# Kernel tuning notes

Measured on AMD Instinct MI355X. Metric: run time of the kernel, lower is better.

## Reference

```python
import jax, jax.numpy as jnp
import numpy as np

B, S, H, Dh = 16, 577, 16, 64
D = H * Dh
DT = 0.01      # resonance_kwargs['dt']
BETA = 4.0     # inverse temperature for phase-coherence readout


def setup_inputs() -> dict:
    key = jax.random.key(0)
    ks = jax.random.split(key, 12)
    n = lambda k, shape, s: jax.random.normal(k, shape, jnp.float32) * s
    return {
        'x': n(ks[0], (B, S, D), 1.0),
        'Wq': n(ks[1], (H, Dh, Dh), 0.08), 'bq': jnp.zeros((H, Dh), jnp.float32),
        'Wk': n(ks[2], (H, Dh, Dh), 0.08), 'bk': jnp.zeros((H, Dh), jnp.float32),
        'Wv': n(ks[3], (H, Dh, Dh), 0.08), 'bv': jnp.zeros((H, Dh), jnp.float32),
        'Womega': n(ks[4], (H, Dh), 0.08), 'bomega': jnp.zeros((H,), jnp.float32),
        'Wtheta': n(ks[5], (H, Dh), 0.08), 'btheta': jnp.zeros((H,), jnp.float32),
        'mu': jnp.ones((H,), jnp.float32),                      # Stuart-Landau growth rate
        'kappa': jnp.full((H,), 0.5, jnp.float32),              # coupling strength
        'alpha': jnp.full((H,), 0.1, jnp.float32),              # Sakaguchi phase lag
        'mix_logit': jnp.full((H,), float(np.log(9.0)), jnp.float32),  # sigmoid -> 0.9 hybrid_mix_init
        'band_logits': jnp.zeros((H, 4), jnp.float32),          # spectral gating, 4 bands
        'Wo': n(ks[6], (D, D), 0.02), 'bo': jnp.zeros((D,), jnp.float32),
        'n_sim_steps': 10,
    }


def reference(x, Wq, bq, Wk, bk, Wv, bv, Womega, bomega, Wtheta, btheta,
              mu, kappa, alpha, mix_logit, band_logits, Wo, bo, n_sim_steps):
    b, s, dm = x.shape
    h, dh = Wq.shape[0], Wq.shape[1]
    # split into per-head slices: [B, H, S, dh]
    xh = x.reshape(b, s, h, dh).transpose(0, 2, 1, 3)
    xh = jnp.nan_to_num(xh, nan=0.0, posinf=0.0, neginf=0.0)
    q = jnp.einsum('bhsd,hde->bhse', xh, Wq) + bq[None, :, None, :]
    k = jnp.einsum('bhsd,hde->bhse', xh, Wk) + bk[None, :, None, :]
    v = jnp.einsum('bhsd,hde->bhse', xh, Wv) + bv[None, :, None, :]
    scale = 1.0 / jnp.sqrt(jnp.float32(dh))
    K = jnp.einsum('bhse,bhte->bhst', q, k) * scale            # coupling kernel / vanilla scores
    # per-token natural frequency and initial phase
    omega = jnp.einsum('bhsd,hd->bhs', xh, Womega) + bomega[None, :, None]
    theta0 = jnp.einsum('bhsd,hd->bhs', xh, Wtheta) + btheta[None, :, None]
    zr0, zi0 = jnp.cos(theta0), jnp.sin(theta0)                # z = r e^{i theta}, r0 = 1
    ca = jnp.cos(alpha)[None, :, None]
    sa = jnp.sin(alpha)[None, :, None]
    Kc = (kappa[None, :, None, None] / s) * K                  # normalized coupling matrix
    mu_b = mu[None, :, None]
    # Stuart-Landau + Kuramoto-Sakaguchi vector field:
    # dz = (mu - |z|^2 + i*omega) z + e^{-i alpha} (Kc @ z)
    def f(zr, zi):
        ur = jnp.einsum('bhst,bht->bhs', Kc, zr)
        ui = jnp.einsum('bhst,bht->bhs', Kc, zi)
        cr = ca * ur + sa * ui
        ci = ca * ui - sa * ur
        g = mu_b - (zr * zr + zi * zi)
        return g * zr - omega * zi + cr, g * zi + omega * zr + ci
    # Heun (predictor-corrector) integration, n_sim_steps steps
    def step(carry, _):
        zr, zi = carry
        d1r, d1i = f(zr, zi)
        d2r, d2i = f(zr + DT * d1r, zi + DT * d1i)
        return (zr + 0.5 * DT * (d1r + d2r), zi + 0.5 * DT * (d1i + d2i)), None
    (zr, zi), _ = jax.lax.scan(step, (zr0, zi0), None, length=n_sim_steps)
    # phase-coherence readout: Re(z_i conj(z_j)) = r_i r_j cos(theta_i - theta_j)
    coher = jnp.einsum('bhs,bht->bhst', zr, zr) + jnp.einsum('bhs,bht->bhst', zi, zi)
    A_res = jax.nn.softmax(BETA * coher, axis=-1)
    # spectral gating of V: 4 bands over the head dim
    gate = jax.nn.sigmoid(band_logits)                          # [H, 4]
    gate_full = jnp.repeat(gate, dh // gate.shape[1], axis=-1)  # [H, dh]
    y_res = jnp.einsum('bhst,bhtd->bhsd', A_res, v * gate_full[None, :, None, :])
    # vanilla QK^T attention branch (hybrid readout)
    y_van = jnp.einsum('bhst,bhtd->bhsd', jax.nn.softmax(K, axis=-1), v)
    mix = jax.nn.sigmoid(mix_logit)[None, :, None, None]
    y = mix * y_res + (1.0 - mix) * y_van
    y = y.transpose(0, 2, 1, 3).reshape(b, s, dm)
    return y @ Wo + bo                                          # base_attn dense/out_proj
```

## Files before the change

kernel.cpp:

```cpp
#include <hip/hip_runtime.h>
#include <hip/hip_bf16.h>

#define S_ 577
#define B_ 16
#define H_ 16
#define DH 64
#define DM 1024
#define BH_ 256
#define DT_ 0.01f
#define BETA_ 4.0f
#define SCALE_ 0.125f
#define SPP 292
#define KPR 293
#define SPW2 37
#define L2E 1.44269504f
#define OFFV2 (4.0f * L2E)
#define OFFR2 (6.0f * L2E)

typedef float f32x4 __attribute__((ext_vector_type(4)));
typedef short s16x8 __attribute__((ext_vector_type(8)));
typedef short s16x4 __attribute__((ext_vector_type(4)));

__device__ inline short f2bf(float x) {
    unsigned b = __builtin_bit_cast(unsigned, x);
    b += 0x7fffu + ((b >> 16) & 1u);
    return (short)(b >> 16);
}
__device__ inline float bf2f(short s) {
    unsigned u = ((unsigned)(unsigned short)s) << 16;
    return __builtin_bit_cast(float, u);
}
__device__ inline float ex2(float x) {
    float r;
    asm("v_exp_f32 %0, %1" : "=v"(r) : "v"(x));
    return r;
}
__device__ inline int vswz(int row) { return (((row >> 3) ^ row) & 7) << 3; }

__global__ __launch_bounds__(512) void k_proj(
    const float* __restrict__ x,
    const float* __restrict__ Wq, const float* __restrict__ bq,
    const float* __restrict__ Wk, const float* __restrict__ bk,
    const float* __restrict__ Wv, const float* __restrict__ bv,
    const float* __restrict__ Wom, const float* __restrict__ bom,
    const float* __restrict__ Wth, const float* __restrict__ bth,
    short* __restrict__ qh, short* __restrict__ kh, short* __restrict__ vh,
    float* __restrict__ om, float* __restrict__ zp)
{
    __shared__ __align__(16) short WqT[64*64], WkT[64*64], WvT[64*64];
    __shared__ __align__(16) short X_l[128*64];
    __shared__ float Wom_l[64], Wth_l[64];

    int bh = blockIdx.x, b = bh >> 4, h = bh & 15;
    int tid = threadIdx.x, w = tid >> 6, lane = tid & 63;
    int c = lane & 15, g = lane >> 4;

    {
        int d = tid >> 3, e0 = (tid & 7) << 3;
        const float* pq = Wq + (size_t)h*4096 + d*64 + e0;
        const float* pk = Wk + (size_t)h*4096 + d*64 + e0;
        const float* pv = Wv + (size_t)h*4096 + d*64 + e0;
        float4 q0 = *(const float4*)pq, q1 = *(const float4*)(pq + 4);
        float4 k0 = *(const float4*)pk, k1 = *(const float4*)(pk + 4);
        float4 v0 = *(const float4*)pv, v1 = *(const float4*)(pv + 4);
        float qv[8] = {q0.x,q0.y,q0.z,q0.w,q1.x,q1.y,q1.z,q1.w};
        float kv[8] = {k0.x,k0.y,k0.z,k0.w,k1.x,k1.y,k1.z,k1.w};
        float vv[8] = {v0.x,v0.y,v0.z,v0.w,v1.x,v1.y,v1.z,v1.w};
        #pragma unroll
        for (int j = 0; j < 8; ++j) {
            int e = e0 + j;
            int off = e*64 + (d ^ ((e&7)<<3));
            WqT[off] = f2bf(qv[j]);
            WkT[off] = f2bf(kv[j]);
            WvT[off] = f2bf(vv[j]);
        }
    }
    if (tid < 64) { Wom_l[tid] = Wom[h*64 + tid]; Wth_l[tid] = Wth[h*64 + tid]; }

    float bqv[4], bkv[4], bvv[4];
    #pragma unroll
    for (int e4 = 0; e4 < 4; ++e4) {
        bqv[e4] = bq[h*64 + e4*16 + c];
        bkv[e4] = bk[h*64 + e4*16 + c];
        bvv[e4] = bv[h*64 + e4*16 + c];
    }
    float bomv = bom[h], bthv = bth[h];

    const size_t xbase = (size_t)b*S_*DM + (size_t)h*DH;

    for (int t5 = 0; t5 < 5; ++t5) {
        int s0 = t5 * 128;
        __syncthreads();
        #pragma unroll
        for (int i = 0; i < 2; ++i) {
            int cid = tid + 512*i;
            int row = cid >> 3, ch = cid & 7;
            int s = s0 + row;
            float xv[8];
            if (s < S_) {
                const float* px = x + xbase + (size_t)s*DM + ch*8;
                float4 a0 = *(const float4*)px, a1 = *(const float4*)(px + 4);
                xv[0]=a0.x; xv[1]=a0.y; xv[2]=a0.z; xv[3]=a0.w;
                xv[4]=a1.x; xv[5]=a1.y; xv[6]=a1.z; xv[7]=a1.w;
                #pragma unroll
                for (int j = 0; j < 8; ++j) if (!isfinite(xv[j])) xv[j] = 0.f;
            } else {
                #pragma unroll
                for (int j = 0; j < 8; ++j) xv[j] = 0.f;
            }
            s16x8 xb;
            #pragma unroll
            for (int j = 0; j < 8; ++j) xb[j] = f2bf(xv[j]);
            *(s16x8*)&X_l[row*64 + ((ch*8) ^ ((row&7)<<3))] = xb;
            float po = 0.f, pt = 0.f;
            #pragma unroll
            for (int j = 0; j < 8; ++j) {
                po = fmaf(xv[j], Wom_l[ch*8 + j], po);
                pt = fmaf(xv[j], Wth_l[ch*8 + j], pt);
            }
            po += __shfl_xor(po, 1, 64); pt += __shfl_xor(pt, 1, 64);
            po += __shfl_xor(po, 2, 64); pt += __shfl_xor(pt, 2, 64);
            po += __shfl_xor(po, 4, 64); pt += __shfl_xor(pt, 4, 64);
            if (ch == 0 && s < S_) {
                om[(size_t)bh*S_ + s] = po + bomv;
                float si, co;
                sincosf(pt + bthv, &si, &co);
                reinterpret_cast<float2*>(zp)[(size_t)bh*S_ + s] = make_float2(co, si);
            }
        }
        __syncthreads();
        int arow = w*16 + c;
        s16x8 xa0 = *(const s16x8*)&X_l[arow*64 + ((g*8)      ^ ((arow&7)<<3))];
        s16x8 xa1 = *(const s16x8*)&X_l[arow*64 + ((g*8 + 32) ^ ((arow&7)<<3))];

        const short* WT[3] = {WqT, WkT, WvT};
        short* dst[3] = {qh, kh, vh};
        #pragma unroll
        for (int o = 0; o < 3; ++o) {
            f32x4 acc[4];
            #pragma unroll
            for (int e4 = 0; e4 < 4; ++e4) {
                int brow = e4*16 + c;
                s16x8 b0 = *(const s16x8*)&WT[o][brow*64 + ((g*8)      ^ ((brow&7)<<3))];
                s16x8 b1 = *(const s16x8*)&WT[o][brow*64 + ((g*8 + 32) ^ ((brow&7)<<3))];
                f32x4 a = {0.f,0.f,0.f,0.f};
                a = __builtin_amdgcn_mfma_f32_16x16x32_bf16(xa0, b0, a, 0, 0, 0);
                a = __builtin_amdgcn_mfma_f32_16x16x32_bf16(xa1, b1, a, 0, 0, 0);
                acc[e4] = a;
            }
            float* bias = (o == 0) ? bqv : (o == 1) ? bkv : bvv;
            #pragma unroll
            for (int r = 0; r < 4; ++r) {
                int s = s0 + w*16 + 4*g + r;
                if (s < S_) {
                    s16x4 pk;
                    pk[0] = f2bf(acc[0][r] + bias[0]);
                    pk[1] = f2bf(acc[1][r] + bias[1]);
                    pk[2] = f2bf(acc[2][r] + bias[2]);
                    pk[3] = f2bf(acc[3][r] + bias[3]);
                    *(s16x4*)(dst[o] + (size_t)bh*S_*DH + (size_t)s*DH + c*4) = pk;
                }
            }
        }
    }
}

__global__ __launch_bounds__(1024) void k_ode(
    const short* __restrict__ qh, const short* __restrict__ kh,
    const float* __restrict__ om,
    const float* __restrict__ mu, const float* __restrict__ kappa,
    const float* __restrict__ alpha, const int* __restrict__ nsim,
    float* __restrict__ zp)
{
    __shared__ __align__(16) unsigned kp_l[64*KPR];
    __shared__ __align__(16) short    q_l[S_*64];
    __shared__ __align__(16) float2   z_l[584];
    __shared__ __align__(16) float2   z1_l[584];
    __shared__ __align__(16) float2   kz_s[8][64];

    int bh = blockIdx.x, h = bh & 15;
    int tid = threadIdx.x, w = tid >> 6, lane = tid & 63;
    const short* kg = kh + (size_t)bh*S_*DH;
    const short* qg = qh + (size_t)bh*S_*DH;
    float2* zpg = reinterpret_cast<float2*>(zp) + (size_t)bh*S_;
    const float* omg = om + (size_t)bh*S_;

    for (int i = tid; i < 584; i += 1024) {
        z_l[i] = (i < S_) ? zpg[i] : make_float2(0.f, 0.f);
        z1_l[i] = make_float2(0.f, 0.f);
    }
    {
        int e0 = (tid & 7) * 8;
        for (int sp = tid >> 3; sp < SPP; sp += 128) {
            int sA = 2*sp, sB = 2*sp + 1;
            s16x8 ka = {0,0,0,0,0,0,0,0}, kb = ka;
            if (sA < S_) ka = *(const s16x8*)(kg + (size_t)sA*DH + e0);
            if (sB < S_) kb = *(const s16x8*)(kg + (size_t)sB*DH + e0);
            #pragma unroll
            for (int j = 0; j < 8; ++j)
                kp_l[(e0+j)*KPR + sp] =
                    ((unsigned)(unsigned short)ka[j]) |
                    (((unsigned)(unsigned short)kb[j]) << 16);
        }
    }
    for (int cid = tid; cid < S_*8; cid += 1024) {
        int s = cid >> 3, c = cid & 7;
        s16x8 v = *(const s16x8*)(qg + (size_t)s*DH + c*8);
        *(s16x8*)&q_l[s*64 + ((c*8) ^ ((s&7)<<3))] = v;
    }
    int i8 = lane >> 3, d0 = (lane & 7) << 3;
    int s0 = w * SPW2;
    float om_r[5];
    #pragma unroll
    for (int m2 = 0; m2 < 5; ++m2) {
        int li = i8 + 8*m2, s = s0 + li;
        om_r[m2] = (li < SPW2 && s < S_) ? omg[s] : 0.f;
    }
    float ca = cosf(alpha[h]), sa = sinf(alpha[h]);
    float muv = mu[h];
    float cc = kappa[h] * SCALE_ / (float)S_;
    int NT = nsim[0];
    int sp0 = (w * SPP) >> 4, spE = ((w + 1) * SPP) >> 4;
    __syncthreads();

    for (int ev = 0; ev < 2*NT; ++ev) {
        bool second = ev & 1;
        const float2* zin = second ? z1_l : z_l;
        float ar = 0.f, ai = 0.f, br = 0.f, bi = 0.f;
        for (int sp = sp0; sp < spE; ++sp) {
            unsigned kv = kp_l[lane*KPR + sp];
            float4 zz = *reinterpret_cast<const float4*>(&zin[2*sp]);
            float klo = __builtin_bit_cast(float, kv << 16);
            float khi = __builtin_bit_cast(float, kv & 0xffff0000u);
            ar = fmaf(klo, zz.x, ar); ai = fmaf(klo, zz.y, ai);
            br = fmaf(khi, zz.z, br); bi = fmaf(khi, zz.w, bi);
        }
        float2 part = make_float2(ar + br, ai + bi);
        if (w < 8) kz_s[w][lane] = part;
        __syncthreads();
        if (w >= 8) {
            float2 t = kz_s[w - 8][lane];
            t.x += part.x; t.y += part.y;
            kz_s[w - 8][lane] = t;
        }
        __syncthreads();
        float sr = 0.f, si = 0.f;
        #pragma unroll
        for (int w2 = 0; w2 < 8; ++w2) {
            float2 t = kz_s[w2][lane];
            sr += t.x; si += t.y;
        }
        float kzr[8], kzi[8];
        #pragma unroll
        for (int j = 0; j < 8; ++j) {
            kzr[j] = __shfl(sr, d0 + j, 64);
            kzi[j] = __shfl(si, d0 + j, 64);
        }
        #pragma unroll
        for (int m2 = 0; m2 < 5; ++m2) {
            int li = i8 + 8*m2, s = s0 + li;
            bool act = (li < SPW2) && (s < S_);
            int sq = (s <= S_-1) ? s : S_-1;
            s16x8 qv = *(const s16x8*)&q_l[sq*64 + (d0 ^ ((sq&7)<<3))];
            float ur = 0.f, ui = 0.f;
            #pragma unroll
            for (int j = 0; j < 8; ++j) {
                float qf = bf2f(qv[j]);
                ur = fmaf(qf, kzr[j], ur);
                ui = fmaf(qf, kzi[j], ui);
            }
            #pragma unroll
            for (int mm = 1; mm < 8; mm <<= 1) {
                ur += __shfl_xor(ur, mm, 64);
                ui += __shfl_xor(ui, mm, 64);
            }
            if (act && d0 == 0) {
                float2 z = zin[s];
                float urc = cc*ur, uic = cc*ui;
                float cr = ca*urc + sa*uic;
                float ci = ca*uic - sa*urc;
                float g = muv - (z.x*z.x + z.y*z.y);
                float dr = fmaf(g, z.x, fmaf(-om_r[m2], z.y, cr));
                float di = fmaf(g, z.y, fmaf( om_r[m2], z.x, ci));
                float2 zb = z_l[s];
                if (!second) {
                    z1_l[s] = make_float2(fmaf(DT_, dr, z.x), fmaf(DT_, di, z.y));
                    z_l[s]  = make_float2(fmaf(0.5f*DT_, dr, zb.x), fmaf(0.5f*DT_, di, zb.y));
                } else {
                    z_l[s]  = make_float2(fmaf(0.5f*DT_, dr, zb.x), fmaf(0.5f*DT_, di, zb.y));
                }
            }
        }
        __syncthreads();
    }
    for (int i = tid; i < S_; i += 1024) zpg[i] = z_l[i];
}

__global__ __launch_bounds__(512) void k_attn(
    const short* __restrict__ qh, const short* __restrict__ kh,
    const short* __restrict__ vh, const float* __restrict__ zp,
    const float* __restrict__ mix_logit, const float* __restrict__ band_logits,
    short* __restrict__ yh)
{
    __shared__ short q_l[128*64];
    __shared__ short P1_l[8][1024];
    __shared__ short k_l2[64*64];
    __shared__ short vT_l[64*64];
    __shared__ float2 zs_l[128];
    __shared__ float2 zt_l[64];

    int blk = blockIdx.x;
    int bh = blk / 5, rc = blk - bh*5;
    int b = bh >> 4, h = bh & 15;
    int r0 = rc * 128;
    int tid = threadIdx.x, w = tid >> 6, lane = tid & 63;
    int c = lane & 15, g = lane >> 4;

    const short* qg = qh + (size_t)bh*S_*DH;
    const short* kg = kh + (size_t)bh*S_*DH;
    const short* vg = vh + (size_t)bh*S_*DH;
    const float2* zpg = (const float2*)zp + (size_t)bh*S_;

    #pragma unroll
    for (int i = 0; i < 2; ++i) {
        int cid = tid + 512*i;
        int row = cid >> 3, ch = cid & 7;
        int s = r0 + row;
        s16x8 val = {0,0,0,0,0,0,0,0};
        if (s < S_) val = *(const s16x8*)(qg + (size_t)s*DH + ch*8);
        *(s16x8*)&q_l[row*64 + ((ch*8) ^ ((row&7)<<3))] = val;
    }
    if (tid < 128) {
        float2 z = (r0 + tid < S_) ? zpg[r0 + tid] : make_float2(0.f,0.f);
        zs_l[tid] = make_float2(z.x*(BETA_*L2E), z.y*(BETA_*L2E));
    }
    __syncthreads();

    s16x8 qf0, qf1;
    {
        int row = w*16 + c;
        qf0 = *(const s16x8*)&q_l[row*64 + ((g*8)      ^ ((row&7)<<3))];
        qf1 = *(const s16x8*)&q_l[row*64 + ((g*8 + 32) ^ ((row&7)<<3))];
    }
    float2 zsr[4];
    #pragma unroll
    for (int r = 0; r < 4; ++r) zsr[r] = zs_l[w*16 + (g<<2) + r];

    f32x4 accv[4], accr[4];
    float Z_v[4], Z_r[4];
    #pragma unroll
    for (int i = 0; i < 4; ++i) {
        accv[i] = (f32x4){0.f,0.f,0.f,0.f};
        accr[i] = (f32x4){0.f,0.f,0.f,0.f};
        Z_v[i] = 0.f; Z_r[i] = 0.f;
    }

    short* P0 = &q_l[w << 10];
    short* P1 = &P1_l[w][0];

    for (int tt = 0; tt < 10; ++tt) {
        int t0g = tt * 64;
        __syncthreads();
        {
            int row = tid >> 3, ch = tid & 7;
            int t = t0g + row;
            s16x8 val = {0,0,0,0,0,0,0,0};
            if (t < S_) val = *(const s16x8*)(kg + (size_t)t*DH + ch*8);
            *(s16x8*)&k_l2[row*64 + ((ch*8) ^ ((row&7)<<3))] = val;
        }
        {
            int tloc = tid >> 3, d0 = (tid & 7) << 3;
            int pt = ((tloc & 15) << 2) + (tloc >> 4);
            s16x8 vv = {0,0,0,0,0,0,0,0};
            if (t0g + tloc < S_) vv = *(const s16x8*)(vg + (size_t)(t0g+tloc)*DH + d0);
            #pragma unroll
            for (int j = 0; j < 8; ++j) {
                int sc = d0 + j;
                int te = ((sc & 3) << 4) + (sc >> 2);
                vT_l[te*64 + (pt ^ vswz(te))] = vv[j];
            }
        }
        if (tid < 64) zt_l[tid] = (t0g + tid < S_) ? zpg[t0g + tid] : make_float2(0.f,0.f);
        __syncthreads();

        f32x4 sv[4], sr4[4];
        #pragma unroll
        for (int sub = 0; sub < 4; ++sub) {
            int row = sub*16 + c;
            s16x8 kf0 = *(const s16x8*)&k_l2[row*64 + ((g*8)      ^ ((c&7)<<3))];
            s16x8 kf1 = *(const s16x8*)&k_l2[row*64 + ((g*8 + 32) ^ ((c&7)<<3))];
            f32x4 a = {0.f,0.f,0.f,0.f};
            a = __builtin_amdgcn_mfma_f32_16x16x32_bf16(qf0, kf0, a, 0, 0, 0);
            a = __builtin_amdgcn_mfma_f32_16x16x32_bf16(qf1, kf1, a, 0, 0, 0);
            sv[sub] = a * (SCALE_ * L2E) - OFFV2;
        }
        #pragma unroll
        for (int sub = 0; sub < 4; ++sub) {
            float2 zt = zt_l[sub*16 + c];
            #pragma unroll
            for (int r = 0; r < 4; ++r)
                sr4[sub][r] = fmaf(zsr[r].x, zt.x, fmaf(zsr[r].y, zt.y, -OFFR2));
        }
        if (t0g + 64 > S_) {
            #pragma unroll
            for (int sub = 0; sub < 4; ++sub)
                if (t0g + sub*16 + c >= S_) {
                    #pragma unroll
                    for (int r = 0; r < 4; ++r) { sv[sub][r] = -1e30f; sr4[sub][r] = -1e30f; }
                }
        }

        #pragma unroll
        for (int r = 0; r < 4; ++r) {
            int sl = (g<<2) + r;
            int pco = sl*64 + ((c*4) ^ ((sl&7)<<3));
            s16x4 pk0, pk1;
            float sumv = 0.f, sumr = 0.f;
            #pragma unroll
            for (int sub = 0; sub < 4; ++sub) {
                float pv = ex2(sv[sub][r]);
                float pr = ex2(sr4[sub][r]);
                sumv += pv; sumr += pr;
                pk0[sub] = f2bf(pv);
                pk1[sub] = f2bf(pr);
            }
            *(s16x4*)&P0[pco] = pk0;
            *(s16x4*)&P1[pco] = pk1;
            Z_v[r] += sumv;
            Z_r[r] += sumr;
        }

        #pragma unroll
        for (int hh = 0; hh < 2; ++hh) {
            int kc = g*8 + 32*hh;
            int po = c*64 + (kc ^ ((c&7)<<3));
            s16x8 pa_v = *(const s16x8*)&P0[po];
            s16x8 pa_r = *(const s16x8*)&P1[po];
            #pragma unroll
            for (int d = 0; d < 4; ++d) {
                int row = d*16 + c;
                s16x8 vf = *(const s16x8*)&vT_l[row*64 + (kc ^ vswz(row))];
                accv[d] = __builtin_amdgcn_mfma_f32_16x16x32_bf16(pa_v, vf, accv[d], 0, 0, 0);
                accr[d] = __builtin_amdgcn_mfma_f32_16x16x32_bf16(pa_r, vf, accr[d], 0, 0, 0);
            }
        }
    }

    #pragma unroll
    for (int mm = 1; mm < 16; mm <<= 1) {
        #pragma unroll
        for (int r = 0; r < 4; ++r) {
            Z_v[r] += __shfl_xor(Z_v[r], mm, 64);
            Z_r[r] += __shfl_xor(Z_r[r], mm, 64);
        }
    }

    float mixv = 1.f/(1.f + __expf(-mix_logit[h]));
    #pragma unroll
    for (int d = 0; d < 4; ++d) {
        float gate = 1.f/(1.f + __expf(-band_logits[h*4 + d]));
        #pragma unroll
        for (int r = 0; r < 4; ++r) {
            int s = r0 + w*16 + (g<<2) + r;
            if (s < S_) {
                float val = mixv*gate*(accr[d][r]/Z_r[r]) + (1.f-mixv)*(accv[d][r]/Z_v[r]);
                yh[(size_t)b*S_*DM + (size_t)s*DM + h*DH + d*16 + c] = f2bf(val);
            }
        }
    }
}

__global__ __launch_bounds__(256) void k_cvt(
    const float* __restrict__ Wo, short* __restrict__ Bt)
{
    __shared__ short tl[64][65];
    int k0 = blockIdx.x * 64, n0 = blockIdx.y * 64;
    int tid = threadIdx.x;
    int r = tid >> 2, cb = (tid & 3) * 16;
    #pragma unroll
    for (int j4 = 0; j4 < 4; ++j4) {
        float4 v = *reinterpret_cast<const float4*>(Wo + (size_t)(k0+r)*1024 + n0 + cb + j4*4);
        tl[r][cb + j4*4 + 0] = f2bf(v.x);
        tl[r][cb + j4*4 + 1] = f2bf(v.y);
        tl[r][cb + j4*4 + 2] = f2bf(v.z);
        tl[r][cb + j4*4 + 3] = f2bf(v.w);
    }
    __syncthreads();
    s16x8 v0, v1;
    #pragma unroll
    for (int j = 0; j < 8; ++j) { v0[j] = tl[cb+j][r]; v1[j] = tl[cb+8+j][r]; }
    *(s16x8*)(Bt + (size_t)(n0+r)*1024 + k0 + cb)     = v0;
    *(s16x8*)(Bt + (size_t)(n0+r)*1024 + k0 + cb + 8) = v1;
}

__global__ __launch_bounds__(256) void k_gemm(
    const short* __restrict__ A, const short* __restrict__ Bt,
    const float* __restrict__ bias, float* __restrict__ out)
{
    const int M = B_ * S_;
    __shared__ short A_l[128*64];
    __shared__ short B_l[128*64];
    int m0 = blockIdx.x * 128, n0 = blockIdx.y * 128;
    int tid = threadIdx.x, w = tid >> 6, lane = tid & 63;
    int c = lane & 15, g = lane >> 4;
    int mb = (w & 1) * 64, nb = (w >> 1) * 64;
    f32x4 acc[4][4];
    #pragma unroll
    for (int i = 0; i < 4; ++i)
        #pragma unroll
        for (int j = 0; j < 4; ++j) acc[i][j] = (f32x4){0.f,0.f,0.f,0.f};
    for (int k0 = 0; k0 < 1024; k0 += 64) {
        __syncthreads();
        #pragma unroll
        for (int i = 0; i < 4; ++i) {
            int cid = tid + 256*i;
            int row = cid >> 3, ch = cid & 7;
            int m = m0 + row;
            s16x8 av = {0,0,0,0,0,0,0,0};
            if (m < M) av = *(const s16x8*)(A + (size_t)m*1024 + k0 + ch*8);
            *(s16x8*)&A_l[row*64 + ((ch*8) ^ ((row&7)<<3))] = av;
            s16x8 bv = *(const s16x8*)(Bt + (size_t)(n0+row)*1024 + k0 + ch*8);
            *(s16x8*)&B_l[row*64 + ((ch*8) ^ ((row&7)<<3))] = bv;
        }
        __syncthreads();
        s16x8 af[4][2], bf[4][2];
        #pragma unroll
        for (int i = 0; i < 4; ++i) {
            int ra = mb + i*16 + c;
            af[i][0] = *(const s16x8*)&A_l[ra*64 + ((g*8)      ^ ((c&7)<<3))];
            af[i][1] = *(const s16x8*)&A_l[ra*64 + ((g*8 + 32) ^ ((c&7)<<3))];
            int rb = nb + i*16 + c;
            bf[i][0] = *(const s16x8*)&B_l[rb*64 + ((g*8)      ^ ((c&7)<<3))];
            bf[i][1] = *(const s16x8*)&B_l[rb*64 + ((g*8 + 32) ^ ((c&7)<<3))];
        }
        #pragma unroll
        for (int i = 0; i < 4; ++i)
            #pragma unroll
            for (int j = 0; j < 4; ++j) {
                acc[i][j] = __builtin_amdgcn_mfma_f32_16x16x32_bf16(af[i][0], bf[j][0], acc[i][j], 0, 0, 0);
                acc[i][j] = __builtin_amdgcn_mfma_f32_16x16x32_bf16(af[i][1], bf[j][1], acc[i][j], 0, 0, 0);
            }
    }
    #pragma unroll
    for (int j = 0; j < 4; ++j) {
        float bv = bias[n0 + nb + j*16 + c];
        #pragma unroll
        for (int i = 0; i < 4; ++i)
            #pragma unroll
            for (int r = 0; r < 4; ++r) {
                int m = m0 + mb + i*16 + 4*g + r;
                if (m < M) out[(size_t)m*1024 + n0 + nb + j*16 + c] = acc[i][j][r] + bv;
            }
    }
}

extern "C" void kernel_launch(void* const* d_in, const int* in_sizes, int n_in,
                              void* d_out, int out_size, void* d_ws, size_t ws_size,
                              hipStream_t stream)
{
    const float* x   = (const float*)d_in[0];
    const float* Wq  = (const float*)d_in[1];
    const float* bq  = (const float*)d_in[2];
    const float* Wk  = (const float*)d_in[3];
    const float* bk  = (const float*)d_in[4];
    const float* Wv  = (const float*)d_in[5];
    const float* bv  = (const float*)d_in[6];
    const float* Wom = (const float*)d_in[7];
    const float* bom = (const float*)d_in[8];
    const float* Wth = (const float*)d_in[9];
    const float* bth = (const float*)d_in[10];
    const float* mu  = (const float*)d_in[11];
    const float* kap = (const float*)d_in[12];
    const float* alp = (const float*)d_in[13];
    const float* mix = (const float*)d_in[14];
    const float* bl  = (const float*)d_in[15];
    const float* Wo  = (const float*)d_in[16];
    const float* bo  = (const float*)d_in[17];
    const int* nsim  = (const int*)d_in[18];

    float* ws = (float*)d_ws;
    const size_t QKV = (size_t)BH_ * S_ * DH;
    float* qf = ws;
    float* kf = qf + QKV;
    float* om = kf + QKV;
    float* zp = om + (size_t)BH_*S_;
    short* qh = (short*)(zp + (size_t)2*BH_*S_);
    short* kh = qh + QKV;
    short* vh = kh + QKV;
    short* yh  = (short*)qf;
    short* WoT = (short*)kf;
    float* outf = (float*)d_out;

    k_proj<<<BH_, 512, 0, stream>>>(x, Wq, bq, Wk, bk, Wv, bv, Wom, bom, Wth, bth,
                                    qh, kh, vh, om, zp);
    k_ode<<<BH_, 1024, 0, stream>>>(qh, kh, om, mu, kap, alp, nsim, zp);
    k_cvt<<<dim3(16,16), 256, 0, stream>>>(Wo, WoT);
    k_attn<<<BH_*5, 512, 0, stream>>>(qh, kh, vh, zp, mix, bl, yh);
    dim3 gg(73, 8);
    k_gemm<<<gg, 256, 0, stream>>>(yh, WoT, bo, outf);
}
```

Before: 326.0 us.

## Keep K and Q operands in registers for the ODE kernel instead of LDS

The ODE kernel no longer stages packed K and swizzled Q in shared memory. Each wave loads its 19 K pairs and its Q rows straight from global memory into registers, and the inner loops are fully unrolled. The cross-lane broadcast of the K·z sums now goes through a small LDS vector read as float4 loads, replacing 16 shuffles per evaluation. This cuts LDS traffic and LDS footprint in the serial 20-evaluation loop, at the cost of more VGPRs in a 1024-thread block and a strided 2-byte global gather for K at setup.

```diff
diff --git a/kernel.cpp b/kernel.cpp
--- a/kernel.cpp
+++ b/kernel.cpp
@@ -10,9 +10,8 @@
 #define DT_ 0.01f
 #define BETA_ 4.0f
 #define SCALE_ 0.125f
-#define SPP 292
-#define KPR 293
 #define SPW2 37
+#define PPW 19
 #define L2E 1.44269504f
 #define OFFV2 (4.0f * L2E)
 #define OFFR2 (6.0f * L2E)
@@ -172,11 +171,10 @@
     const float* __restrict__ alpha, const int* __restrict__ nsim,
     float* __restrict__ zp)
 {
-    __shared__ __align__(16) unsigned kp_l[64*KPR];
-    __shared__ __align__(16) short    q_l[S_*64];
-    __shared__ __align__(16) float2   z_l[584];
-    __shared__ __align__(16) float2   z1_l[584];
-    __shared__ __align__(16) float2   kz_s[8][64];
+    __shared__ __align__(16) float2 z_l[608];
+    __shared__ __align__(16) float2 z1_l[608];
+    __shared__ __align__(16) float2 kz_s[8][64];
+    __shared__ __align__(16) float2 kzv[64];
 
     int bh = blockIdx.x, h = bh & 15;
     int tid = threadIdx.x, w = tid >> 6, lane = tid & 63;
@@ -185,53 +183,48 @@
     float2* zpg = reinterpret_cast<float2*>(zp) + (size_t)bh*S_;
     const float* omg = om + (size_t)bh*S_;
 
-    for (int i = tid; i < 584; i += 1024) {
+    for (int i = tid; i < 608; i += 1024) {
         z_l[i] = (i < S_) ? zpg[i] : make_float2(0.f, 0.f);
         z1_l[i] = make_float2(0.f, 0.f);
     }
-    {
-        int e0 = (tid & 7) * 8;
-        for (int sp = tid >> 3; sp < SPP; sp += 128) {
-            int sA = 2*sp, sB = 2*sp + 1;
-            s16x8 ka = {0,0,0,0,0,0,0,0}, kb = ka;
-            if (sA < S_) ka = *(const s16x8*)(kg + (size_t)sA*DH + e0);
-            if (sB < S_) kb = *(const s16x8*)(kg + (size_t)sB*DH + e0);
-            #pragma unroll
-            for (int j = 0; j < 8; ++j)
-                kp_l[(e0+j)*KPR + sp] =
-                    ((unsigned)(unsigned short)ka[j]) |
-                    (((unsigned)(unsigned short)kb[j]) << 16);
-        }
-    }
-    for (int cid = tid; cid < S_*8; cid += 1024) {
-        int s = cid >> 3, c = cid & 7;
-        s16x8 v = *(const s16x8*)(qg + (size_t)s*DH + c*8);
-        *(s16x8*)&q_l[s*64 + ((c*8) ^ ((s&7)<<3))] = v;
+
+    int sp0 = w * PPW;
+    unsigned k_reg[PPW];
+    #pragma unroll
+    for (int j = 0; j < PPW; ++j) {
+        int sA = 2*(sp0 + j), sB = sA + 1;
+        unsigned lo = (sA < S_) ? (unsigned)(unsigned short)kg[(size_t)sA*DH + lane] : 0u;
+        unsigned hi = (sB < S_) ? (unsigned)(unsigned short)kg[(size_t)sB*DH + lane] : 0u;
+        k_reg[j] = lo | (hi << 16);
     }
     int i8 = lane >> 3, d0 = (lane & 7) << 3;
     int s0 = w * SPW2;
+    s16x8 q_reg[5];
     float om_r[5];
     #pragma unroll
     for (int m2 = 0; m2 < 5; ++m2) {
         int li = i8 + 8*m2, s = s0 + li;
-        om_r[m2] = (li < SPW2 && s < S_) ? omg[s] : 0.f;
+        bool ok = (li < SPW2) && (s < S_);
+        s16x8 v = {0,0,0,0,0,0,0,0};
+        if (ok) v = *(const s16x8*)(qg + (size_t)s*DH + d0);
+        q_reg[m2] = v;
+        om_r[m2] = ok ? omg[s] : 0.f;
     }
     float ca = cosf(alpha[h]), sa = sinf(alpha[h]);
     float muv = mu[h];
     float cc = kappa[h] * SCALE_ / (float)S_;
     int NT = nsim[0];
-    int sp0 = (w * SPP) >> 4, spE = ((w + 1) * SPP) >> 4;
     __syncthreads();
 
     for (int ev = 0; ev < 2*NT; ++ev) {
         bool second = ev & 1;
         const float2* zin = second ? z1_l : z_l;
         float ar = 0.f, ai = 0.f, br = 0.f, bi = 0.f;
-        for (int sp = sp0; sp < spE; ++sp) {
-            unsigned kv = kp_l[lane*KPR + sp];
-            float4 zz = *reinterpret_cast<const float4*>(&zin[2*sp]);
-            float klo = __builtin_bit_cast(float, kv << 16);
-            float khi = __builtin_bit_cast(float, kv & 0xffff0000u);
+        #pragma unroll
+        for (int j = 0; j < PPW; ++j) {
+            float4 zz = *reinterpret_cast<const float4*>(&zin[2*(sp0 + j)]);
+            float klo = __builtin_bit_cast(float, k_reg[j] << 16);
+            float khi = __builtin_bit_cast(float, k_reg[j] & 0xffff0000u);
             ar = fmaf(klo, zz.x, ar); ai = fmaf(klo, zz.y, ai);
             br = fmaf(khi, zz.z, br); bi = fmaf(khi, zz.w, bi);
         }
@@ -244,28 +237,29 @@
             kz_s[w - 8][lane] = t;
         }
         __syncthreads();
-        float sr = 0.f, si = 0.f;
-        #pragma unroll
-        for (int w2 = 0; w2 < 8; ++w2) {
-            float2 t = kz_s[w2][lane];
-            sr += t.x; si += t.y;
-        }
-        float kzr[8], kzi[8];
-        #pragma unroll
-        for (int j = 0; j < 8; ++j) {
-            kzr[j] = __shfl(sr, d0 + j, 64);
-            kzi[j] = __shfl(si, d0 + j, 64);
-        }
+        {
+            float sr = 0.f, si = 0.f;
+            #pragma unroll
+            for (int w2 = 0; w2 < 8; ++w2) {
+                float2 t = kz_s[w2][lane];
+                sr += t.x; si += t.y;
+            }
+            kzv[lane] = make_float2(sr, si);
+        }
+        float4 kza = *reinterpret_cast<const float4*>(&kzv[d0]);
+        float4 kzb = *reinterpret_cast<const float4*>(&kzv[d0 + 2]);
+        float4 kzc = *reinterpret_cast<const float4*>(&kzv[d0 + 4]);
+        float4 kzd = *reinterpret_cast<const float4*>(&kzv[d0 + 6]);
+        float kzr[8] = {kza.x, kza.z, kzb.x, kzb.z, kzc.x, kzc.z, kzd.x, kzd.z};
+        float kzi[8] = {kza.y, kza.w, kzb.y, kzb.w, kzc.y, kzc.w, kzd.y, kzd.w};
         #pragma unroll
         for (int m2 = 0; m2 < 5; ++m2) {
             int li = i8 + 8*m2, s = s0 + li;
             bool act = (li < SPW2) && (s < S_);
-            int sq = (s <= S_-1) ? s : S_-1;
-            s16x8 qv = *(const s16x8*)&q_l[sq*64 + (d0 ^ ((sq&7)<<3))];
             float ur = 0.f, ui = 0.f;
             #pragma unroll
             for (int j = 0; j < 8; ++j) {
-                float qf = bf2f(qv[j]);
+                float qf = bf2f(q_reg[m2][j]);
                 ur = fmaf(qf, kzr[j], ur);
                 ui = fmaf(qf, kzi[j], ui);
             }
```

New measurement: 626.9 us. +92.3%, slower.
